# Optimization experiments

Measured on AMD Instinct MI355X. Metric: run time of the kernel, lower is better.

The kernel has to match this reference:

```python
import jax, jax.numpy as jnp
import numpy as np

B, L, H = 2, 2048, 1024
NH, HD = 16, 64  # n_heads, head_size


def setup_inputs() -> dict:
    key = jax.random.key(0)
    ks = jax.random.split(key, 12)
    scale = 1.0 / np.sqrt(H)
    inp = {
        "hidden_states": jax.random.normal(ks[0], (B, L, H), dtype=jnp.float32),
        "tau": jax.random.uniform(ks[1], (B, 1), dtype=jnp.float32) + 0.5,
        "delta": jax.random.normal(ks[2], (B, L), dtype=jnp.float32) * 0.1,
        "Wq": jax.random.normal(ks[3], (H, H), dtype=jnp.float32) * scale,
        "bq": jnp.zeros((H,), dtype=jnp.float32),
        "Wk": jax.random.normal(ks[4], (H, H), dtype=jnp.float32) * scale,
        "bk": jnp.zeros((H,), dtype=jnp.float32),
        "Wv": jax.random.normal(ks[5], (H, H), dtype=jnp.float32) * scale,
        "bv": jnp.zeros((H,), dtype=jnp.float32),
        "Wo": jax.random.normal(ks[6], (H, H), dtype=jnp.float32) * scale,
        "bo": jnp.zeros((H,), dtype=jnp.float32),
    }
    return inp


def _split_heads(x):
    # [B, L, H] -> [B, NH, L, HD]
    return x.reshape(B, L, NH, HD).transpose(0, 2, 1, 3)


def reference(hidden_states, tau, delta, Wq, bq, Wk, bk, Wv, bv, Wo, bo):
    q = _split_heads(hidden_states @ Wq.T + bq)
    k = _split_heads(hidden_states @ Wk.T + bk)
    v = _split_heads(hidden_states @ Wv.T + bv)
    tau_b = tau[:, :, None, None]          # [B,1,1,1]
    delta_b = delta[:, None, None, :]      # [B,1,1,L]
    scores = jnp.einsum('bhqd,bhkd->bhqk', q, k) * tau_b + delta_b
    scores = scores / np.sqrt(HD)
    attn = jax.nn.softmax(scores, axis=-1)  # dropout = identity (eval mode)
    ctx = jnp.einsum('bhqk,bhkd->bhqd', attn, v)
    ctx = ctx.transpose(0, 2, 1, 3).reshape(B, L, H)
    return ctx @ Wo.T + bo
```

## Files before the change

### kernel.cpp

```cpp
#include <hip/hip_runtime.h>

#define B_ 2
#define L_ 2048
#define H_ 1024
#define NH_ 16
#define HD_ 64

using short8 = __attribute__((__ext_vector_type__(8))) short;
using f32x4 = __attribute__((__ext_vector_type__(4))) float;
using f32x16 = __attribute__((__ext_vector_type__(16))) float;
typedef unsigned short u16;
typedef unsigned int u32;

__device__ __forceinline__ u16 f2bf(float f) {
  union { float f; unsigned u; } x{f};
  unsigned u = x.u;
  u = u + 0x7FFFu + ((u >> 16) & 1u);
  return (u16)(u >> 16);
}

__device__ __forceinline__ void gld16(const void* g, void* l) {
  __builtin_amdgcn_global_load_lds(
      (const __attribute__((address_space(1))) void*)g,
      (__attribute__((address_space(3))) void*)l, 16, 0, 0);
}

#define MFMA16(a, b, c) __builtin_amdgcn_mfma_f32_16x16x32_bf16((a), (b), (c), 0, 0, 0)
#define MFMA32(a, b, c) __builtin_amdgcn_mfma_f32_32x32x16_bf16((a), (b), (c), 0, 0, 0)

__global__ void cast_all(const float* __restrict__ hs, const float* __restrict__ Wq,
                         const float* __restrict__ Wk, const float* __restrict__ Wv,
                         const float* __restrict__ Wo, const float* __restrict__ delta,
                         u16* __restrict__ dst, u16* __restrict__ dscb) {
  const int t = blockIdx.x * 256 + threadIdx.x;
  const int i = t * 4;
  const float* src;
  int off;
  if (i < 4194304) {
    src = hs; off = i;
  } else {
    const int j = i - 4194304;
    const int w = j >> 20;
    off = j & 1048575;
    src = (w == 0) ? Wq : (w == 1) ? Wk : (w == 2) ? Wv : Wo;
  }
  float4 v = *(const float4*)(src + off);
  *(ushort4*)(dst + i) = make_ushort4(f2bf(v.x), f2bf(v.y), f2bf(v.z), f2bf(v.w));
  if (t < 4096) dscb[t] = f2bf(delta[t] * 0.18033688011112042f);
}

__global__ __launch_bounds__(512) void gemm_qkv192(
    const u16* __restrict__ A, const u16* __restrict__ W,
    const float* __restrict__ bq, const float* __restrict__ bk, const float* __restrict__ bv,
    const float* __restrict__ tau,
    u16* __restrict__ qg, u16* __restrict__ kg, u16* __restrict__ vTg) {
  __shared__ u16 As[2][256 * 64];
  __shared__ u16 Bs[2][192 * 64];
  const int tid = threadIdx.x;
  const int lane = tid & 63;
  const int wid = tid >> 6;
  const int wr = wid >> 2;
  const int wc = wid & 3;
  const int orig = blockIdx.y * 16 + blockIdx.x;
  const int wg = (orig & 7) * 32 + (orig >> 3);
  const int m0 = (wg & 15) * 256;
  const int n0 = (wg >> 4) * 192;

  const int srow = tid >> 3;
  const int sg = tid & 7;

#define STAGEQ(slot, t_)                                                                \
  {                                                                                     \
    const int kt64 = (t_) * 64;                                                         \
    _Pragma("unroll") for (int li = 0; li < 4; li++) {                                  \
      const int row = li * 64 + srow;                                                   \
      const int gsrc = sg ^ (row & 7);                                                  \
      gld16(A + (size_t)(m0 + row) * 1024 + kt64 + gsrc * 8,                            \
            (char*)As[slot] + li * 8192 + wid * 1024 + lane * 16);                      \
    }                                                                                   \
    _Pragma("unroll") for (int li = 0; li < 3; li++) {                                  \
      const int row = li * 64 + srow;                                                   \
      const int gsrc = sg ^ (row & 7);                                                  \
      gld16(W + (size_t)(n0 + row) * 1024 + kt64 + gsrc * 8,                            \
            (char*)Bs[slot] + li * 8192 + wid * 1024 + lane * 16);                      \
    }                                                                                   \
  }

  f32x4 acc[8][3] = {};

  STAGEQ(0, 0);
  STAGEQ(1, 1);

  for (int t = 0; t < 16; t++) {
    if (t >= 1 && t + 1 < 16) STAGEQ((t + 1) & 1, t + 1);
    if (t + 1 < 16) {
      asm volatile("s_waitcnt vmcnt(7)" ::: "memory");
    } else {
      asm volatile("s_waitcnt vmcnt(0)" ::: "memory");
    }
    asm volatile("s_barrier" ::: "memory");
    const u16* Ab = As[t & 1];
    const u16* Bb = Bs[t & 1];
    short8 bf[3];
#pragma unroll
    for (int q = 0; q < 4; q++) {
      const int mh = q & 1, ks = q >> 1;
      const int g0 = ks * 4 + (lane >> 4);
      if (mh == 0) {
#pragma unroll
        for (int ni = 0; ni < 3; ni++) {
          const int r = wc * 48 + ni * 16 + (lane & 15);
          bf[ni] = *(const short8*)((const char*)Bb + r * 128 + ((g0 ^ (r & 7)) << 4));
        }
      }
      short8 af[4];
#pragma unroll
      for (int mi = 0; mi < 4; mi++) {
        const int r = wr * 128 + (mh * 4 + mi) * 16 + (lane & 15);
        af[mi] = *(const short8*)((const char*)Ab + r * 128 + ((g0 ^ (r & 7)) << 4));
      }
      __builtin_amdgcn_s_setprio(1);
#pragma unroll
      for (int mi = 0; mi < 4; mi++)
#pragma unroll
        for (int ni = 0; ni < 3; ni++)
          acc[mh * 4 + mi][ni] = MFMA16(af[mi], bf[ni], acc[mh * 4 + mi][ni]);
      __builtin_amdgcn_s_setprio(0);
      asm volatile("s_barrier" ::: "memory");
    }
  }

  const int b_blk = m0 >> 11;
  const float tauv = tau[b_blk] * 0.18033688011112042f;
#pragma unroll
  for (int ni = 0; ni < 3; ni++) {
    const int nbase = n0 + wc * 48 + ni * 16;
    const int which = nbase >> 10;
    const int n = nbase + (lane & 15);
    const int nn = n & 1023;
    const int h = nn >> 6, d = nn & 63;
    const float* bias = which == 0 ? bq : (which == 1 ? bk : bv);
    const float bb = bias[nn];
    const float scl = which == 0 ? tauv : 1.0f;
#pragma unroll
    for (int mi = 0; mi < 8; mi++) {
      const int mb = m0 + wr * 128 + mi * 16 + ((lane >> 4) << 2);
      const int b = mb >> 11;
      const int lq = mb & 2047;
      if (which == 2) {
        ushort4 pk = make_ushort4(f2bf(acc[mi][ni][0] + bb), f2bf(acc[mi][ni][1] + bb),
                                  f2bf(acc[mi][ni][2] + bb), f2bf(acc[mi][ni][3] + bb));
        *(ushort4*)&vTg[((size_t)(b * NH_ + h) * HD_ + d) * L_ + lq] = pk;
      } else {
        u16* dst = which == 0 ? qg : kg;
#pragma unroll
        for (int r = 0; r < 4; r++)
          dst[((size_t)(b * NH_ + h) * L_ + lq + r) * HD_ + d] = f2bf((acc[mi][ni][r] + bb) * scl);
      }
    }
  }
}

__global__ __launch_bounds__(512) void attn(
    const u16* __restrict__ qg, const u16* __restrict__ kg, const u16* __restrict__ vTg,
    const u16* __restrict__ dscb, u16* __restrict__ ctxg) {
  __shared__ u16 lds[2][16384];
  const int tid = threadIdx.x;
  const int lane = tid & 63;
  const int wv = tid >> 6;
  const int lane31 = lane & 31;
  const int hi = lane >> 5;
  const int orig = blockIdx.x;
  const int wgid = (orig & 7) * 32 + (orig >> 3);
  const int bh = wgid >> 3;
  const int qblk = wgid & 7;
  const int b = bh >> 4;
  const int h = bh & 15;
  const int q0 = qblk * 256 + wv * 32;
  const u16* qb = qg + (size_t)bh * L_ * HD_;
  const u16* kb = kg + (size_t)bh * L_ * HD_;
  const u16* vb = vTg + (size_t)bh * HD_ * L_;
  const u16* dbb = dscb + (size_t)b * L_;

  short8 qf[4];
#pragma unroll
  for (int ks = 0; ks < 4; ks++)
    qf[ks] = *(const short8*)&qb[(size_t)(q0 + lane31) * 64 + ks * 16 + hi * 8];

  union U8 { u32 u[4]; short8 s; };
  U8 onesu;
  const u32 ow = (lane31 == 0) ? 0x3F803F80u : 0u;
  onesu.u[0] = ow; onesu.u[1] = ow; onesu.u[2] = ow; onesu.u[3] = ow;
  const short8 onesf = onesu.s;
  U8 onesbu;
  onesbu.u[0] = (hi == 0) ? 0x00003F80u : 0u;
  onesbu.u[1] = 0; onesbu.u[2] = 0; onesbu.u[3] = 0;
  const short8 onesB = onesbu.s;

  f32x16 acc[2] = {};
  f32x16 accl = {};
  float mrun = -__builtin_inff();

#define STAGE(bp_, j0_)                                                                   \
  {                                                                                       \
    u16* bp = (bp_);                                                                      \
    _Pragma("unroll") for (int s = 0; s < 2; s++) {                                       \
      const int i = 2 * wv + s;                                                           \
      const int kt = i >> 2, ks = i & 3;                                                  \
      gld16(kb + (size_t)((j0_) + kt * 32 + lane31) * 64 + ks * 16 + hi * 8,              \
            bp + i * 512 + lane * 8);                                                     \
    }                                                                                     \
    _Pragma("unroll") for (int s = 0; s < 2; s++) {                                       \
      const int i = 2 * wv + s;                                                           \
      const int kt = i >> 2, dt = (i >> 1) & 1, ks2 = i & 1;                              \
      gld16(vb + (size_t)(dt * 32 + lane31) * L_ + (j0_) + kt * 32 + ks2 * 16 + hi * 8,   \
            bp + (16 + i) * 512 + lane * 8);                                              \
    }                                                                                     \
  }

  STAGE(lds[0], 0);
  __syncthreads();

  for (int t = 0; t < 16; t++) {
    const int j0 = t * 128;
    if (t + 1 < 16) STAGE(lds[(t + 1) & 1], j0 + 128);
    const u16* bp = lds[t & 1];

    f32x16 sp[4];
    __builtin_amdgcn_s_setprio(1);
#pragma unroll
    for (int kt = 0; kt < 4; kt++) {
      U8 df;
      df.u[0] = (hi == 0) ? (u32)dbb[j0 + kt * 32 + lane31] : 0u;
      df.u[1] = 0; df.u[2] = 0; df.u[3] = 0;
      f32x16 s = MFMA32(df.s, onesB, f32x16{});
#pragma unroll
      for (int ks = 0; ks < 4; ks++) {
        short8 kf = *(const short8*)&bp[(kt * 4 + ks) * 512 + lane * 8];
        s = MFMA32(kf, qf[ks], s);
      }
      sp[kt] = s;
    }
    __builtin_amdgcn_s_setprio(0);

    float tm[4];
#pragma unroll
    for (int r = 0; r < 4; r++) {
      float a0 = fmaxf(fmaxf(sp[0][r], sp[0][4 + r]), fmaxf(sp[0][8 + r], sp[0][12 + r]));
      float a1 = fmaxf(fmaxf(sp[1][r], sp[1][4 + r]), fmaxf(sp[1][8 + r], sp[1][12 + r]));
      float a2 = fmaxf(fmaxf(sp[2][r], sp[2][4 + r]), fmaxf(sp[2][8 + r], sp[2][12 + r]));
      float a3 = fmaxf(fmaxf(sp[3][r], sp[3][4 + r]), fmaxf(sp[3][8 + r], sp[3][12 + r]));
      tm[r] = fmaxf(fmaxf(a0, a1), fmaxf(a2, a3));
    }
    float pmax = fmaxf(fmaxf(tm[0], tm[1]), fmaxf(tm[2], tm[3]));
    pmax = fmaxf(pmax, __shfl_xor(pmax, 32));
    if (!__all(pmax - mrun <= 11.5f)) {
      float mnew = fmaxf(mrun, pmax);
      float al = __builtin_amdgcn_exp2f(mrun - mnew);
      mrun = mnew;
      accl[0] *= al;
#pragma unroll
      for (int dt = 0; dt < 2; dt++)
#pragma unroll
        for (int r = 0; r < 16; r++) acc[dt][r] *= al;
    }

#pragma unroll
    for (int kt = 0; kt < 4; kt++) {
#pragma unroll
      for (int r = 0; r < 16; r++) sp[kt][r] = __builtin_amdgcn_exp2f(sp[kt][r] - mrun);
      u32 pk[8];
#pragma unroll
      for (int i = 0; i < 8; i++)
        asm("v_cvt_pk_bf16_f32 %0, %1, %2" : "=v"(pk[i]) : "v"(sp[kt][2 * i]), "v"(sp[kt][2 * i + 1]));
      asm volatile("v_permlane32_swap_b32 %0, %1" : "+v"(pk[0]), "+v"(pk[2]));
      asm volatile("v_permlane32_swap_b32 %0, %1" : "+v"(pk[1]), "+v"(pk[3]));
      asm volatile("v_permlane32_swap_b32 %0, %1" : "+v"(pk[4]), "+v"(pk[6]));
      asm volatile("v_permlane32_swap_b32 %0, %1" : "+v"(pk[5]), "+v"(pk[7]));
      __builtin_amdgcn_s_setprio(1);
#pragma unroll
      for (int ks2 = 0; ks2 < 2; ks2++) {
        U8 pf;
        pf.u[0] = pk[ks2 * 4 + 0]; pf.u[1] = pk[ks2 * 4 + 1];
        pf.u[2] = pk[ks2 * 4 + 2]; pf.u[3] = pk[ks2 * 4 + 3];
#pragma unroll
        for (int dt = 0; dt < 2; dt++) {
          short8 vf = *(const short8*)&bp[(16 + kt * 4 + dt * 2 + ks2) * 512 + lane * 8];
          acc[dt] = MFMA32(vf, pf.s, acc[dt]);
        }
        accl = MFMA32(onesf, pf.s, accl);
      }
      __builtin_amdgcn_s_setprio(0);
    }
    __syncthreads();
  }

  u16* tw = (u16*)lds + wv * 2048;
  const float l0 = accl[0];
  const float l1 = __shfl_xor(l0, 32);
  const float inv = 1.0f / (hi ? l1 : l0);
#pragma unroll
  for (int dt = 0; dt < 2; dt++)
#pragma unroll
    for (int g = 0; g < 4; g++) {
      ushort4 w4 = make_ushort4(f2bf(acc[dt][g * 4 + 0] * inv), f2bf(acc[dt][g * 4 + 1] * inv),
                                f2bf(acc[dt][g * 4 + 2] * inv), f2bf(acc[dt][g * 4 + 3] * inv));
      const int d0 = dt * 32 + g * 8 + hi * 4;
      const int byte = (lane31 * 128 + d0 * 2) ^ ((lane31 & 15) << 3);
      *(ushort4*)((char*)tw + byte) = w4;
    }
  asm volatile("s_waitcnt lgkmcnt(0)" ::: "memory");
  const size_t obase = ((size_t)b * L_ + q0) * 1024 + h * 64;
#pragma unroll
  for (int i = 0; i < 16; i++) {
    const int qr = 2 * i + hi;
    const int byte = (qr * 128 + lane31 * 4) ^ ((qr & 15) << 3);
    const u32 val = *(const u32*)((const char*)tw + byte);
    *(u32*)&ctxg[obase + (size_t)qr * 1024 + lane31 * 2] = val;
  }
}

__global__ __launch_bounds__(256) void gemm_out128(
    const u16* __restrict__ A, const u16* __restrict__ W,
    const float* __restrict__ bo, float* __restrict__ out) {
  __shared__ u16 As[2][128 * 64];
  __shared__ u16 Bs[2][128 * 64];
  const int tid = threadIdx.x;
  const int lane = tid & 63;
  const int wid = tid >> 6;
  const int wr = wid >> 1;
  const int wc = wid & 1;
  const int orig = blockIdx.y * 8 + blockIdx.x;
  const int wg = (orig & 7) * 32 + (orig >> 3);
  const int m0 = (wg & 31) * 128;
  const int n0 = (wg >> 5) * 128;

  const int srow = tid >> 3;
  const int sg = tid & 7;

#define STAGEO(slot, t_)                                                                \
  {                                                                                     \
    const int kt64 = (t_) * 64;                                                         \
    _Pragma("unroll") for (int li = 0; li < 4; li++) {                                  \
      const int row = li * 32 + srow;                                                   \
      const int gsrc = sg ^ (row & 7);                                                  \
      gld16(A + (size_t)(m0 + row) * 1024 + kt64 + gsrc * 8,                            \
            (char*)As[slot] + li * 4096 + wid * 1024 + lane * 16);                      \
      gld16(W + (size_t)(n0 + row) * 1024 + kt64 + gsrc * 8,                            \
            (char*)Bs[slot] + li * 4096 + wid * 1024 + lane * 16);                      \
    }                                                                                   \
  }

  f32x4 acc[4][4] = {};

  STAGEO(0, 0);
  STAGEO(1, 1);

  for (int t = 0; t < 16; t++) {
    if (t >= 1 && t + 1 < 16) STAGEO((t + 1) & 1, t + 1);
    if (t + 1 < 16) {
      asm volatile("s_waitcnt vmcnt(8)" ::: "memory");
    } else {
      asm volatile("s_waitcnt vmcnt(0)" ::: "memory");
    }
    asm volatile("s_barrier" ::: "memory");
    const u16* Ab = As[t & 1];
    const u16* Bb = Bs[t & 1];
    short8 bf[4];
#pragma unroll
    for (int q = 0; q < 4; q++) {
      const int mh = q & 1, ks = q >> 1;
      const int g0 = ks * 4 + (lane >> 4);
      if (mh == 0) {
#pragma unroll
        for (int ni = 0; ni < 4; ni++) {
          const int r = wc * 64 + ni * 16 + (lane & 15);
          bf[ni] = *(const short8*)((const char*)Bb + r * 128 + ((g0 ^ (r & 7)) << 4));
        }
      }
      short8 af[2];
#pragma unroll
      for (int mi = 0; mi < 2; mi++) {
        const int r = wr * 64 + (mh * 2 + mi) * 16 + (lane & 15);
        af[mi] = *(const short8*)((const char*)Ab + r * 128 + ((g0 ^ (r & 7)) << 4));
      }
      __builtin_amdgcn_s_setprio(1);
#pragma unroll
      for (int mi = 0; mi < 2; mi++)
#pragma unroll
        for (int ni = 0; ni < 4; ni++)
          acc[mh * 2 + mi][ni] = MFMA16(af[mi], bf[ni], acc[mh * 2 + mi][ni]);
      __builtin_amdgcn_s_setprio(0);
      asm volatile("s_barrier" ::: "memory");
    }
  }

#pragma unroll
  for (int ni = 0; ni < 4; ni++) {
    const int n = n0 + wc * 64 + ni * 16 + (lane & 15);
    const float bb = bo[n];
#pragma unroll
    for (int mi = 0; mi < 4; mi++) {
      const int mb = m0 + wr * 64 + mi * 16 + ((lane >> 4) << 2);
#pragma unroll
      for (int r = 0; r < 4; r++)
        out[(size_t)(mb + r) * 1024 + n] = acc[mi][ni][r] + bb;
    }
  }
}

extern "C" void kernel_launch(void* const* d_in, const int* in_sizes, int n_in,
                              void* d_out, int out_size, void* d_ws, size_t ws_size,
                              hipStream_t stream) {
  const float* hs = (const float*)d_in[0];
  const float* tau = (const float*)d_in[1];
  const float* delta = (const float*)d_in[2];
  const float* Wq = (const float*)d_in[3];
  const float* bq = (const float*)d_in[4];
  const float* Wk = (const float*)d_in[5];
  const float* bk = (const float*)d_in[6];
  const float* Wv = (const float*)d_in[7];
  const float* bv = (const float*)d_in[8];
  const float* Wo = (const float*)d_in[9];
  const float* bo = (const float*)d_in[10];
  float* out = (float*)d_out;

  u16* ws = (u16*)d_ws;
  u16* hsb  = ws;
  u16* wqkv = ws + 4194304;
  u16* wob  = ws + 7340032;
  u16* qg   = ws + 8388608;
  u16* kg   = ws + 12582912;
  u16* vTg  = ws + 16777216;
  u16* ctxg = ws + 20971520;
  u16* dscb = ws + 25165824;

  cast_all<<<8192, 256, 0, stream>>>(hs, Wq, Wk, Wv, Wo, delta, ws, dscb);

  gemm_qkv192<<<dim3(16, 16), 512, 0, stream>>>(hsb, wqkv, bq, bk, bv, tau, qg, kg, vTg);
  attn<<<256, 512, 0, stream>>>(qg, kg, vTg, dscb, ctxg);
  gemm_out128<<<dim3(8, 32), 256, 0, stream>>>(ctxg, wob, bo, out);
}
```

Baseline: 134.5 us.

## Give each wave private K/V staging with vmcnt pipelining, drop block barriers

Replaces the shared 128-key tile that the whole block loads cooperatively with per-wave 32-key K/V tiles, double-buffered in LDS. Each wave uses s_waitcnt vmcnt and no longer waits at __syncthreads each iteration. The intent is to remove block-wide synchronisation stalls and let waves run independently. The cost is that every wave now loads the same K/V data separately, multiplying global/L2 traffic by eight, and the loop has smaller 32-key steps with more per-iteration softmax overhead.

```diff
diff --git a/kernel.cpp b/kernel.cpp
--- a/kernel.cpp
+++ b/kernel.cpp
@@ -164,7 +164,7 @@
 __global__ __launch_bounds__(512) void attn(
     const u16* __restrict__ qg, const u16* __restrict__ kg, const u16* __restrict__ vTg,
     const u16* __restrict__ dscb, u16* __restrict__ ctxg) {
-  __shared__ u16 lds[2][16384];
+  __shared__ u16 lds[2][8][4096];
   const int tid = threadIdx.x;
   const int lane = tid & 63;
   const int wv = tid >> 6;
@@ -201,57 +201,47 @@
   f32x16 accl = {};
   float mrun = -__builtin_inff();
 
-#define STAGE(bp_, j0_)                                                                   \
+#define STAGEP(buf_, j_)                                                                  \
   {                                                                                       \
-    u16* bp = (bp_);                                                                      \
-    _Pragma("unroll") for (int s = 0; s < 2; s++) {                                       \
-      const int i = 2 * wv + s;                                                           \
-      const int kt = i >> 2, ks = i & 3;                                                  \
-      gld16(kb + (size_t)((j0_) + kt * 32 + lane31) * 64 + ks * 16 + hi * 8,              \
-            bp + i * 512 + lane * 8);                                                     \
+    u16* bp = &lds[buf_][wv][0];                                                          \
+    _Pragma("unroll") for (int ks = 0; ks < 4; ks++)                                      \
+        gld16(kb + (size_t)((j_) + lane31) * 64 + ks * 16 + hi * 8,                       \
+              bp + ks * 512 + lane * 8);                                                  \
+    _Pragma("unroll") for (int i = 0; i < 4; i++) {                                       \
+      const int dt = i >> 1, ks2 = i & 1;                                                 \
+      gld16(vb + (size_t)(dt * 32 + lane31) * L_ + (j_) + ks2 * 16 + hi * 8,              \
+            bp + (4 + i) * 512 + lane * 8);                                               \
     }                                                                                     \
-    _Pragma("unroll") for (int s = 0; s < 2; s++) {                                       \
-      const int i = 2 * wv + s;                                                           \
-      const int kt = i >> 2, dt = (i >> 1) & 1, ks2 = i & 1;                              \
-      gld16(vb + (size_t)(dt * 32 + lane31) * L_ + (j0_) + kt * 32 + ks2 * 16 + hi * 8,   \
-            bp + (16 + i) * 512 + lane * 8);                                              \
-    }                                                                                     \
-  }
-
-  STAGE(lds[0], 0);
-  __syncthreads();
-
-  for (int t = 0; t < 16; t++) {
-    const int j0 = t * 128;
-    if (t + 1 < 16) STAGE(lds[(t + 1) & 1], j0 + 128);
-    const u16* bp = lds[t & 1];
-
-    f32x16 sp[4];
+  }
+
+  STAGEP(0, 0);
+  STAGEP(1, 32);
+
+  for (int t = 0; t < 64; t++) {
+    if (t < 63) {
+      asm volatile("s_waitcnt vmcnt(8)" ::: "memory");
+    } else {
+      asm volatile("s_waitcnt vmcnt(0)" ::: "memory");
+    }
+    const u16* bp = &lds[t & 1][wv][0];
+    const int j0 = t * 32;
+
+    U8 df;
+    df.u[0] = (hi == 0) ? (u32)dbb[j0 + lane31] : 0u;
+    df.u[1] = 0; df.u[2] = 0; df.u[3] = 0;
     __builtin_amdgcn_s_setprio(1);
-#pragma unroll
-    for (int kt = 0; kt < 4; kt++) {
-      U8 df;
-      df.u[0] = (hi == 0) ? (u32)dbb[j0 + kt * 32 + lane31] : 0u;
-      df.u[1] = 0; df.u[2] = 0; df.u[3] = 0;
-      f32x16 s = MFMA32(df.s, onesB, f32x16{});
-#pragma unroll
-      for (int ks = 0; ks < 4; ks++) {
-        short8 kf = *(const short8*)&bp[(kt * 4 + ks) * 512 + lane * 8];
-        s = MFMA32(kf, qf[ks], s);
-      }
-      sp[kt] = s;
+    f32x16 s = MFMA32(df.s, onesB, f32x16{});
+#pragma unroll
+    for (int ks = 0; ks < 4; ks++) {
+      short8 kf = *(const short8*)&bp[ks * 512 + lane * 8];
+      s = MFMA32(kf, qf[ks], s);
     }
     __builtin_amdgcn_s_setprio(0);
 
     float tm[4];
 #pragma unroll
-    for (int r = 0; r < 4; r++) {
-      float a0 = fmaxf(fmaxf(sp[0][r], sp[0][4 + r]), fmaxf(sp[0][8 + r], sp[0][12 + r]));
-      float a1 = fmaxf(fmaxf(sp[1][r], sp[1][4 + r]), fmaxf(sp[1][8 + r], sp[1][12 + r]));
-      float a2 = fmaxf(fmaxf(sp[2][r], sp[2][4 + r]), fmaxf(sp[2][8 + r], sp[2][12 + r]));
-      float a3 = fmaxf(fmaxf(sp[3][r], sp[3][4 + r]), fmaxf(sp[3][8 + r], sp[3][12 + r]));
-      tm[r] = fmaxf(fmaxf(a0, a1), fmaxf(a2, a3));
-    }
+    for (int r = 0; r < 4; r++)
+      tm[r] = fmaxf(fmaxf(s[r], s[4 + r]), fmaxf(s[8 + r], s[12 + r]));
     float pmax = fmaxf(fmaxf(tm[0], tm[1]), fmaxf(tm[2], tm[3]));
     pmax = fmaxf(pmax, __shfl_xor(pmax, 32));
     if (!__all(pmax - mrun <= 11.5f)) {
@@ -264,38 +254,37 @@
 #pragma unroll
         for (int r = 0; r < 16; r++) acc[dt][r] *= al;
     }
-
-#pragma unroll
-    for (int kt = 0; kt < 4; kt++) {
-#pragma unroll
-      for (int r = 0; r < 16; r++) sp[kt][r] = __builtin_amdgcn_exp2f(sp[kt][r] - mrun);
-      u32 pk[8];
-#pragma unroll
-      for (int i = 0; i < 8; i++)
-        asm("v_cvt_pk_bf16_f32 %0, %1, %2" : "=v"(pk[i]) : "v"(sp[kt][2 * i]), "v"(sp[kt][2 * i + 1]));
-      asm volatile("v_permlane32_swap_b32 %0, %1" : "+v"(pk[0]), "+v"(pk[2]));
-      asm volatile("v_permlane32_swap_b32 %0, %1" : "+v"(pk[1]), "+v"(pk[3]));
-      asm volatile("v_permlane32_swap_b32 %0, %1" : "+v"(pk[4]), "+v"(pk[6]));
-      asm volatile("v_permlane32_swap_b32 %0, %1" : "+v"(pk[5]), "+v"(pk[7]));
-      __builtin_amdgcn_s_setprio(1);
-#pragma unroll
-      for (int ks2 = 0; ks2 < 2; ks2++) {
-        U8 pf;
-        pf.u[0] = pk[ks2 * 4 + 0]; pf.u[1] = pk[ks2 * 4 + 1];
-        pf.u[2] = pk[ks2 * 4 + 2]; pf.u[3] = pk[ks2 * 4 + 3];
-#pragma unroll
-        for (int dt = 0; dt < 2; dt++) {
-          short8 vf = *(const short8*)&bp[(16 + kt * 4 + dt * 2 + ks2) * 512 + lane * 8];
-          acc[dt] = MFMA32(vf, pf.s, acc[dt]);
-        }
-        accl = MFMA32(onesf, pf.s, accl);
-      }
-      __builtin_amdgcn_s_setprio(0);
-    }
-    __syncthreads();
-  }
-
-  u16* tw = (u16*)lds + wv * 2048;
+#pragma unroll
+    for (int r = 0; r < 16; r++) s[r] = __builtin_amdgcn_exp2f(s[r] - mrun);
+    u32 pk[8];
+#pragma unroll
+    for (int i = 0; i < 8; i++)
+      asm("v_cvt_pk_bf16_f32 %0, %1, %2" : "=v"(pk[i]) : "v"(s[2 * i]), "v"(s[2 * i + 1]));
+    asm volatile("v_permlane32_swap_b32 %0, %1" : "+v"(pk[0]), "+v"(pk[2]));
+    asm volatile("v_permlane32_swap_b32 %0, %1" : "+v"(pk[1]), "+v"(pk[3]));
+    asm volatile("v_permlane32_swap_b32 %0, %1" : "+v"(pk[4]), "+v"(pk[6]));
+    asm volatile("v_permlane32_swap_b32 %0, %1" : "+v"(pk[5]), "+v"(pk[7]));
+
+    __builtin_amdgcn_s_setprio(1);
+#pragma unroll
+    for (int ks2 = 0; ks2 < 2; ks2++) {
+      U8 pf;
+      pf.u[0] = pk[ks2 * 4 + 0]; pf.u[1] = pk[ks2 * 4 + 1];
+      pf.u[2] = pk[ks2 * 4 + 2]; pf.u[3] = pk[ks2 * 4 + 3];
+#pragma unroll
+      for (int dt = 0; dt < 2; dt++) {
+        short8 vf = *(const short8*)&bp[(4 + dt * 2 + ks2) * 512 + lane * 8];
+        acc[dt] = MFMA32(vf, pf.s, acc[dt]);
+      }
+      accl = MFMA32(onesf, pf.s, accl);
+    }
+    __builtin_amdgcn_s_setprio(0);
+
+    __builtin_amdgcn_sched_barrier(0);
+    if (t + 2 < 64) STAGEP(t & 1, j0 + 64);
+  }
+
+  u16* tw = &lds[0][wv][0];
   const float l0 = accl[0];
   const float l1 = __shfl_xor(l0, 32);
   const float inv = 1.0f / (hi ? l1 : l0);
```

Result: slower. 190.2 us (+41.4%).
